# Kernel tuning notes

Hardware: AMD Instinct MI355X
Metric: run time of the kernel (lower is better)

## Reference

```python
import jax, jax.numpy as jnp
import numpy as np

N = 100_000      # nodes
E = 1_600_000    # edges (before self-loops)
IN_DIM = 128
HID = 64
NEG_SLOPE = 0.2  # PyG GATConv default


def gat_layer(x, src, dst, W, att_src, att_dst, bias, heads, out_ch):
    """PyG-style GATConv: messages flow src -> dst, softmax over incoming edges of dst."""
    n = x.shape[0]
    h = (x @ W).reshape(n, heads, out_ch)                 # [N,H,C]
    a_src = jnp.einsum('nhc,hc->nh', h, att_src)          # [N,H]
    a_dst = jnp.einsum('nhc,hc->nh', h, att_dst)          # [N,H]
    e = jax.nn.leaky_relu(a_src[src] + a_dst[dst], NEG_SLOPE)  # [E,H]
    # segment softmax over edges grouped by destination node
    m = jax.ops.segment_max(e, dst, num_segments=n)       # [N,H]
    ex = jnp.exp(e - m[dst])                              # [E,H]
    denom = jax.ops.segment_sum(ex, dst, num_segments=n)  # [N,H]
    alpha = ex / denom[dst]                               # [E,H]
    msg = alpha[:, :, None] * h[src]                      # [E,H,C]
    out = jax.ops.segment_sum(msg, dst, num_segments=n)   # [N,H,C]
    return out.reshape(n, heads * out_ch) + bias


def setup_inputs() -> dict:
    key = jax.random.key(0)
    ks = jax.random.split(key, 12)
    s = 0.1
    x = jax.random.normal(ks[0], (N, IN_DIM), jnp.float32)
    edge_index = jax.random.randint(ks[1], (2, E), 0, N, dtype=jnp.int32)
    # conv1: in_dim -> hidden, heads=2 (concat)
    W1 = jax.random.normal(ks[2], (IN_DIM, 2 * HID), jnp.float32) * s
    att_src1 = jax.random.normal(ks[3], (2, HID), jnp.float32) * s
    att_dst1 = jax.random.normal(ks[4], (2, HID), jnp.float32) * s
    b1 = jnp.zeros((2 * HID,), jnp.float32)
    # conv2: 2*hidden -> 1, heads=1
    W2 = jax.random.normal(ks[5], (2 * HID, 1), jnp.float32) * s
    att_src2 = jax.random.normal(ks[6], (1, 1), jnp.float32) * s
    att_dst2 = jax.random.normal(ks[7], (1, 1), jnp.float32) * s
    b2 = jnp.zeros((1,), jnp.float32)
    return {"x": x, "edge_index": edge_index,
            "W1": W1, "att_src1": att_src1, "att_dst1": att_dst1, "b1": b1,
            "W2": W2, "att_src2": att_src2, "att_dst2": att_dst2, "b2": b2}


def reference(x, edge_index, W1, att_src1, att_dst1, b1, W2, att_src2, att_dst2, b2):
    n = x.shape[0]
    # PyG GATConv default: add self-loops
    loop = jnp.arange(n, dtype=edge_index.dtype)
    src = jnp.concatenate([edge_index[0], loop])
    dst = jnp.concatenate([edge_index[1], loop])
    h = jax.nn.relu(gat_layer(x, src, dst, W1, att_src1, att_dst1, b1, heads=2, out_ch=HID))
    out = gat_layer(h, src, dst, W2, att_src2, att_dst2, b2, heads=1, out_ch=1)
    return jax.nn.sigmoid(out)  # [N,1]
```

## Files before the change

### kernel.cpp

```cpp
#include <hip/hip_runtime.h>
#include <hip/hip_bf16.h>
#include <hip/hip_fp8.h>
#include <hip/hip_fp16.h>

#define NEG 0.2f
#define CAP 48
#define TILE 2048
typedef unsigned int u32;
typedef unsigned short u16;
typedef unsigned char u8;
typedef unsigned long long u64;
typedef __attribute__((ext_vector_type(8))) short s8v;
typedef __attribute__((ext_vector_type(4))) float f4v;
typedef __attribute__((ext_vector_type(2))) float f2v;

__global__ __launch_bounds__(256) void binA_k(const int* __restrict__ ei,
                                              int2* __restrict__ meta,
                                              u64* __restrict__ slabs,
                                              int E, int Etot, int NB, int ntiles){
  __shared__ int bcnt[512], sc[512], bcur[512];
  int tile = blockIdx.x, tid = threadIdx.x;
  int base = tile*TILE;
  int cnt = min(TILE, Etot - base);
  for (int i=tid;i<512;i+=256) bcnt[i]=0;
  __syncthreads();
  int dd[8], ss[8];
  #pragma unroll
  for (int j=0;j<8;j++){
    int i = tid + j*256;
    if (i < cnt){
      int e = base+i;
      int d = (e<E)? ei[E+e] : e-E;
      int s = (e<E)? ei[e]   : d;
      dd[j] = d; ss[j] = s;
      atomicAdd(&bcnt[d>>8], 1);
    } else dd[j] = -1;
  }
  __syncthreads();
  sc[tid]     = bcnt[tid];
  sc[tid+256] = bcnt[tid+256];
  __syncthreads();
  for (int o=1;o<512;o<<=1){
    int i0=tid, i1=tid+256;
    int r0 = (i0>=o)? sc[i0-o]:0;
    int r1 = (i1>=o)? sc[i1-o]:0;
    __syncthreads();
    sc[i0]+=r0; sc[i1]+=r1;
    __syncthreads();
  }
  bcur[tid]     = sc[tid]     - bcnt[tid];
  bcur[tid+256] = sc[tid+256] - bcnt[tid+256];
  __syncthreads();
  for (int b=tid;b<NB;b+=256)
    meta[(size_t)b*ntiles + tile] = make_int2(sc[b]-bcnt[b], bcnt[b]);
  #pragma unroll
  for (int j=0;j<8;j++){
    if (dd[j] >= 0){
      int p = atomicAdd(&bcur[dd[j]>>8], 1);
      slabs[(size_t)base + p] = ((u64)(u32)dd[j] << 32) | (u32)ss[j];
    }
  }
}

__global__ __launch_bounds__(1024) void binB_k(const u64* __restrict__ slabs,
                                               const int2* __restrict__ meta,
                                               const float2* __restrict__ as1,
                                               const float2* __restrict__ ad1,
                                               int* __restrict__ cur,
                                               u32* __restrict__ woff,
                                               u64* __restrict__ combo,
                                               float2* __restrict__ den,
                                               int N, int ntiles){
  __shared__ u64 lcombo[CAP*256];
  __shared__ int lcnt[256], loff[256];
  __shared__ float sden0[256], sden1[256];
  __shared__ float2 sad[256];
  int b = blockIdx.x, tid = threadIdx.x;
  int lo = b<<8;
  int nn = min(256, N-lo);
  if (tid < 256){
    lcnt[tid]=0; sden0[tid]=0.f; sden1[tid]=0.f;
    sad[tid] = (tid<nn)? ad1[lo+tid] : make_float2(0.f,0.f);
  }
  __syncthreads();
  int grp = tid>>3, l8 = tid&7;
  const int2* mrow = meta + (size_t)b*ntiles;
  int2 m = (grp < ntiles)? mrow[grp] : make_int2(0,0);
  for (int t=grp; t<ntiles; t+=128){
    int2 mn = (t+128 < ntiles)? mrow[t+128] : make_int2(0,0);
    const u64* sp = slabs + (size_t)t*TILE + m.x;
    for (int i=l8; i<m.y; i+=8){
      u64 pk = sp[i];
      int d = (int)(pk>>32), s = (int)(u32)pk;
      int dl = d & 255;
      float2 av = as1[s];
      float2 adv = sad[dl];
      float e0 = av.x+adv.x; e0 = (e0>0.f)? e0 : NEG*e0;
      float e1 = av.y+adv.y; e1 = (e1>0.f)? e1 : NEG*e1;
      __half2 hw = __floats2half2_rn(__expf(e0), __expf(e1));
      float2 wr = __half22float2(hw);
      atomicAdd(&sden0[dl], wr.x);
      atomicAdd(&sden1[dl], wr.y);
      int p = atomicAdd(&lcnt[dl], 1);
      u32 wb32 = *(u32*)&hw;
      if (p < CAP) lcombo[p*256 + dl] = ((u64)wb32 << 32) | (u32)s;
    }
    m = mn;
  }
  __syncthreads();
  if (tid < 256){
    lcnt[tid] = min(lcnt[tid], CAP);
    loff[tid] = lcnt[tid];
  }
  __syncthreads();
  for (int o=1;o<256;o<<=1){
    int v = 0;
    if (tid < 256 && tid >= o) v = loff[tid-o];
    __syncthreads();
    if (tid < 256) loff[tid] += v;
    __syncthreads();
  }
  u32 wbase = (u32)b * (256u*CAP);
  {
    int g = tid>>2, q = tid&3;
    int dg  = lcnt[g];
    u32 ob  = wbase + (u32)(loff[g] - dg);
    for (int k=q; k<dg; k+=4)
      combo[(size_t)(ob + (u32)k)] = lcombo[k*256 + g];
  }
  __syncthreads();
  if (tid < nn){
    cur[lo+tid]  = lcnt[tid];
    woff[lo+tid] = wbase + (u32)(loff[tid] - lcnt[tid]);
    den[lo+tid]  = make_float2(sden0[tid], sden1[tid]);
  }
}

__global__ __launch_bounds__(256) void wt_k(const float* __restrict__ W, u16* __restrict__ Wt){
  int g = blockIdx.x*256 + threadIdx.x;
  int k = g >> 7, c = g & 127;
  __hip_bfloat16 b = __float2bfloat16(W[g]);
  Wt[c*128 + k] = *(u16*)&b;
}

__global__ __launch_bounds__(256) void gemm_k(const float* __restrict__ x,
                                              const u16* __restrict__ Wt,
                                              const float* __restrict__ aw_s,
                                              const float* __restrict__ aw_d,
                                              u8*  __restrict__ h1f,
                                              float2* __restrict__ as1,
                                              float2* __restrict__ ad1, int N){
  __shared__ u16 xs[128*136];
  __shared__ u16 ws[128*136];
  int tid = threadIdx.x;
  int rowBase = blockIdx.x * 128;
  #pragma unroll
  for (int i=0;i<16;i++){
    int j = i*256 + tid;
    int c = j >> 5, k4 = j & 31;
    *(uint2*)&ws[c*136 + k4*4] = ((const uint2*)Wt)[j];
  }
  #pragma unroll
  for (int i=0;i<16;i++){
    int j = i*256 + tid;
    int r = j >> 5, c4 = j & 31;
    float4 v = make_float4(0.f,0.f,0.f,0.f);
    if (rowBase + r < N) v = ((const float4*)x)[(size_t)(rowBase+r)*32 + c4];
    __hip_bfloat16 b0=__float2bfloat16(v.x), b1=__float2bfloat16(v.y);
    __hip_bfloat16 b2=__float2bfloat16(v.z), b3=__float2bfloat16(v.w);
    u32 w0 = (u32)*(u16*)&b0 | ((u32)*(u16*)&b1 << 16);
    u32 w1 = (u32)*(u16*)&b2 | ((u32)*(u16*)&b3 << 16);
    *(uint2*)&xs[r*136 + c4*4] = make_uint2(w0, w1);
  }
  __syncthreads();
  int wv = tid >> 6, lane = tid & 63;
  int lr = lane & 15, lk = lane >> 4;
  f4v acc[2][8];
  #pragma unroll
  for (int rt=0;rt<2;rt++)
    #pragma unroll
    for (int ct=0;ct<8;ct++) acc[rt][ct] = (f4v){0.f,0.f,0.f,0.f};
  #pragma unroll
  for (int ks=0; ks<4; ks++){
    int koff = ks*32 + lk*8;
    s8v bfrag[8];
    #pragma unroll
    for (int ct=0; ct<8; ct++)
      bfrag[ct] = *(s8v*)&ws[(ct*16 + lr)*136 + koff];
    #pragma unroll
    for (int rt=0; rt<2; rt++){
      int row = wv*32 + rt*16 + lr;
      s8v afrag = *(s8v*)&xs[row*136 + koff];
      #pragma unroll
      for (int ct=0; ct<8; ct++)
        acc[rt][ct] = __builtin_amdgcn_mfma_f32_16x16x32_bf16(afrag, bfrag[ct], acc[rt][ct], 0,0,0);
    }
  }
  #pragma unroll
  for (int rt=0; rt<2; rt++){
    float lps0[4]={0,0,0,0}, lps1[4]={0,0,0,0}, lpd0[4]={0,0,0,0}, lpd1[4]={0,0,0,0};
    int nodeB = rowBase + wv*32 + rt*16 + lk*4;
    #pragma unroll
    for (int ct=0; ct<8; ct++){
      int ch = ct*16 + lr;
      float aws = aw_s[ch], awd = aw_d[ch];
      #pragma unroll
      for (int reg=0; reg<4; reg++){
        float v = acc[rt][ct][reg];
        if (ct < 4){ lps0[reg] = fmaf(v, aws, lps0[reg]); lpd0[reg] = fmaf(v, awd, lpd0[reg]); }
        else       { lps1[reg] = fmaf(v, aws, lps1[reg]); lpd1[reg] = fmaf(v, awd, lpd1[reg]); }
      }
      int pk01 = __builtin_amdgcn_cvt_pk_fp8_f32(acc[rt][ct][0], acc[rt][ct][1], 0, false);
      int pk23 = __builtin_amdgcn_cvt_pk_fp8_f32(acc[rt][ct][2], acc[rt][ct][3], 0, false);
      if (nodeB + 0 < N) h1f[(size_t)(nodeB+0)*128 + ch] = (u8)(pk01 & 0xff);
      if (nodeB + 1 < N) h1f[(size_t)(nodeB+1)*128 + ch] = (u8)((pk01 >> 8) & 0xff);
      if (nodeB + 2 < N) h1f[(size_t)(nodeB+2)*128 + ch] = (u8)(pk23 & 0xff);
      if (nodeB + 3 < N) h1f[(size_t)(nodeB+3)*128 + ch] = (u8)((pk23 >> 8) & 0xff);
    }
    #pragma unroll
    for (int reg=0; reg<4; reg++){
      float a=lps0[reg], b=lps1[reg], c=lpd0[reg], d=lpd1[reg];
      #pragma unroll
      for (int o=1;o<16;o<<=1){
        a += __shfl_xor(a,o); b += __shfl_xor(b,o);
        c += __shfl_xor(c,o); d += __shfl_xor(d,o);
      }
      int node = nodeB + reg;
      if (lr == 0 && node < N){
        as1[node] = make_float2(a, b);
        ad1[node] = make_float2(c, d);
      }
    }
  }
}

__global__ __launch_bounds__(256) void agg1_k(const uint2* __restrict__ h1f2,
                                              const u64* __restrict__ combo,
                                              const u32* __restrict__ woff,
                                              const float2* __restrict__ den,
                                              const int* __restrict__ cur,
                                              const float4* __restrict__ b1_4,
                                              const float4* __restrict__ W2_4,
                                              float* __restrict__ h2, int N){
  int w = threadIdx.x >> 6, l = threadIdx.x & 63;
  int g = l >> 4, li = l & 15;
  int n = blockIdx.x*16 + w*4 + g;
  if (n >= N) return;
  int deg = min(cur[n], CAP);
  u32 base = woff[n];
  bool hsel = (li >= 8);
  float2 dn = den[n];
  float rd = 1.f / (hsel ? dn.y : dn.x);
  float ac0=0.f,ac1=0.f,ac2=0.f,ac3=0.f,ac4=0.f,ac5=0.f,ac6=0.f,ac7=0.f;
  for (int kk = 0; kk < deg; kk += 8){
    u64 pk[8]; bool vd[8];
    #pragma unroll
    for (int j=0;j<8;j++){
      int idx = kk + j;
      vd[j] = idx < deg;
      pk[j] = combo[(size_t)(base + (u32)(vd[j] ? idx : 0))];
    }
    uint2 hv[8];
    #pragma unroll
    for (int j=0;j<8;j++){
      u32 off = ((u32)(pk[j] & 0xffffffffu) << 4) | (u32)li;
      hv[j] = h1f2[off];
    }
    #pragma unroll
    for (int j=0;j<8;j++){
      u32 wb = (u32)(pk[j] >> 32);
      __half2 hw = *(__half2*)&wb;
      float2 wf = __half22float2(hw);
      float gw = hsel ? wf.y : wf.x;
      gw = vd[j] ? gw : 0.f;
      f2v p0 = __builtin_amdgcn_cvt_pk_f32_fp8((int)hv[j].x, false);
      f2v p1 = __builtin_amdgcn_cvt_pk_f32_fp8((int)hv[j].x, true);
      f2v p2 = __builtin_amdgcn_cvt_pk_f32_fp8((int)hv[j].y, false);
      f2v p3 = __builtin_amdgcn_cvt_pk_f32_fp8((int)hv[j].y, true);
      ac0 = fmaf(gw, p0.x, ac0); ac1 = fmaf(gw, p0.y, ac1);
      ac2 = fmaf(gw, p1.x, ac2); ac3 = fmaf(gw, p1.y, ac3);
      ac4 = fmaf(gw, p2.x, ac4); ac5 = fmaf(gw, p2.y, ac5);
      ac6 = fmaf(gw, p3.x, ac6); ac7 = fmaf(gw, p3.y, ac7);
    }
  }
  float4 bb0 = b1_4[li*2], bb1 = b1_4[li*2+1];
  float4 ww0 = W2_4[li*2], ww1 = W2_4[li*2+1];
  float p = 0.f;
  p = fmaf(fmaxf(fmaf(ac0, rd, bb0.x), 0.f), ww0.x, p);
  p = fmaf(fmaxf(fmaf(ac1, rd, bb0.y), 0.f), ww0.y, p);
  p = fmaf(fmaxf(fmaf(ac2, rd, bb0.z), 0.f), ww0.z, p);
  p = fmaf(fmaxf(fmaf(ac3, rd, bb0.w), 0.f), ww0.w, p);
  p = fmaf(fmaxf(fmaf(ac4, rd, bb1.x), 0.f), ww1.x, p);
  p = fmaf(fmaxf(fmaf(ac5, rd, bb1.y), 0.f), ww1.y, p);
  p = fmaf(fmaxf(fmaf(ac6, rd, bb1.z), 0.f), ww1.z, p);
  p = fmaf(fmaxf(fmaf(ac7, rd, bb1.w), 0.f), ww1.w, p);
  #pragma unroll
  for (int o=1;o<16;o<<=1) p += __shfl_xor(p,o);
  if (li == 0) h2[n] = p;
}

__global__ __launch_bounds__(256) void agg2_k(const float* __restrict__ h2,
                                              const int* __restrict__ cur,
                                              const u32* __restrict__ woff,
                                              const u64* __restrict__ combo,
                                              const float* __restrict__ att_s2,
                                              const float* __restrict__ att_d2,
                                              const float* __restrict__ b2,
                                              float* __restrict__ out, int N){
  int w = threadIdx.x >> 6, l = threadIdx.x & 63;
  int n = blockIdx.x*4 + w;
  if (n >= N) return;
  float as2 = att_s2[0], ad2 = att_d2[0];
  float hd = h2[n]*ad2;
  int deg = min(cur[n], CAP);
  u32 base = woff[n];
  bool v = l < deg;
  int s = (int)(u32)(combo[(size_t)(base + (u32)(v ? l : 0))] & 0xffffffffu);
  float hs = h2[s];
  float e = fmaf(hs, as2, hd); e = (e>0.f)? e : NEG*e;
  float xv = v ? __expf(e) : 0.f;
  float den = xv, wsum = xv*hs;
  #pragma unroll
  for (int o=32;o>0;o>>=1){ den += __shfl_xor(den,o); wsum += __shfl_xor(wsum,o); }
  if (l == 0){
    float z = wsum/den + b2[0];
    out[n] = 1.f/(1.f + __expf(-z));
  }
}

extern "C" void kernel_launch(void* const* d_in, const int* in_sizes, int n_in,
                              void* d_out, int out_size, void* d_ws, size_t ws_size,
                              hipStream_t stream){
  const float* x     = (const float*)d_in[0];
  const int*   ei    = (const int*)d_in[1];
  const float* W1    = (const float*)d_in[2];
  const float* aw_s  = (const float*)d_in[3];
  const float* aw_d  = (const float*)d_in[4];
  const float* b1    = (const float*)d_in[5];
  const float* W2    = (const float*)d_in[6];
  const float* at_s2 = (const float*)d_in[7];
  const float* at_d2 = (const float*)d_in[8];
  const float* b2    = (const float*)d_in[9];
  float* out = (float*)d_out;

  const int N = in_sizes[0]/128;
  const int E = in_sizes[1]/2;
  const int Etot = E + N;
  const int ntiles = (Etot + TILE - 1) / TILE;
  const int NB = (N + 255) >> 8;

  auto align256 = [](size_t v){ return (v + 255) & ~(size_t)255; };
  char* w = (char*)d_ws;
  u8* h1f       = (u8*)w;     w += align256((size_t)N*128);
  float2* as1   = (float2*)w; w += align256((size_t)N*8);
  float2* ad1   = (float2*)w; w += align256((size_t)N*8);
  float* h2     = (float*)w;  w += align256((size_t)N*4);
  int* cur      = (int*)w;    w += align256((size_t)N*4);
  u32* woff     = (u32*)w;    w += align256((size_t)N*4);
  float2* den   = (float2*)w; w += align256((size_t)N*8);
  u16* Wt       = (u16*)w;    w += align256((size_t)128*128*2);
  u64* combo    = (u64*)w;    w += align256((size_t)NB*256*CAP*8);
  u64* slabs    = (u64*)w;    w += align256((size_t)ntiles*TILE*8);
  int2* meta    = (int2*)w;   w += align256((size_t)NB*ntiles*8);

  const int tb = 256;
  binA_k<<<ntiles, tb, 0, stream>>>(ei, meta, slabs, E, Etot, NB, ntiles);
  wt_k<<<64, tb, 0, stream>>>(W1, Wt);
  gemm_k<<<(N+127)/128, tb, 0, stream>>>(x, Wt, aw_s, aw_d, h1f, as1, ad1, N);
  binB_k<<<NB, 1024, 0, stream>>>(slabs, meta, as1, ad1, cur, woff, combo, den, N, ntiles);
  agg1_k<<<(N+15)/16, tb, 0, stream>>>((const uint2*)h1f, combo, woff, den, cur,
                                       (const float4*)b1, (const float4*)W2, h2, N);
  agg2_k<<<(N+3)/4, tb, 0, stream>>>(h2, cur, woff, combo, at_s2, at_d2, b2, out, N);
}
```

Measured before the change: 174.0 us.

## Compute edge attention weights in binning pass, derive softmax denominator in aggregation

The exp-leaky-relu edge weight is now computed in binA_k, which is moved after the GEMM. The weight is packed into the slab word along with the local destination and a 24-bit source index. binB_k becomes a pure scatter into per-node slots, with no as1 gathers, no shared-memory float atomics and no den output. agg1_k sums the denominator from the weights it already reads. This trades shared atomics and a separate den array for an extra random ad1 gather per edge in binA. The denominator now covers only the first CAP edges kept per node, which changes numerics for nodes with more than CAP incoming edges.

```diff
diff --git a/kernel.cpp b/kernel.cpp
--- a/kernel.cpp
+++ b/kernel.cpp
@@ -15,6 +15,8 @@
 typedef __attribute__((ext_vector_type(2))) float f2v;
 
 __global__ __launch_bounds__(256) void binA_k(const int* __restrict__ ei,
+                                              const float2* __restrict__ as1,
+                                              const float2* __restrict__ ad1,
                                               int2* __restrict__ meta,
                                               u64* __restrict__ slabs,
                                               int E, int Etot, int NB, int ntiles){
@@ -36,6 +38,18 @@
       atomicAdd(&bcnt[d>>8], 1);
     } else dd[j] = -1;
   }
+  u32 wreg[8];
+  #pragma unroll
+  for (int j=0;j<8;j++){
+    if (dd[j] >= 0){
+      float2 av = as1[ss[j]];
+      float2 adv = ad1[dd[j]];
+      float e0 = av.x+adv.x; e0 = (e0>0.f)? e0 : NEG*e0;
+      float e1 = av.y+adv.y; e1 = (e1>0.f)? e1 : NEG*e1;
+      __half2 hw = __floats2half2_rn(__expf(e0), __expf(e1));
+      wreg[j] = *(u32*)&hw;
+    }
+  }
   __syncthreads();
   sc[tid]     = bcnt[tid];
   sc[tid+256] = bcnt[tid+256];
@@ -57,31 +71,23 @@
   for (int j=0;j<8;j++){
     if (dd[j] >= 0){
       int p = atomicAdd(&bcur[dd[j]>>8], 1);
-      slabs[(size_t)base + p] = ((u64)(u32)dd[j] << 32) | (u32)ss[j];
+      slabs[(size_t)base + p] = ((u64)wreg[j] << 32) | ((u64)(dd[j]&255) << 24) | (u32)ss[j];
     }
   }
 }
 
 __global__ __launch_bounds__(1024) void binB_k(const u64* __restrict__ slabs,
                                                const int2* __restrict__ meta,
-                                               const float2* __restrict__ as1,
-                                               const float2* __restrict__ ad1,
                                                int* __restrict__ cur,
                                                u32* __restrict__ woff,
                                                u64* __restrict__ combo,
-                                               float2* __restrict__ den,
                                                int N, int ntiles){
   __shared__ u64 lcombo[CAP*256];
   __shared__ int lcnt[256], loff[256];
-  __shared__ float sden0[256], sden1[256];
-  __shared__ float2 sad[256];
   int b = blockIdx.x, tid = threadIdx.x;
   int lo = b<<8;
   int nn = min(256, N-lo);
-  if (tid < 256){
-    lcnt[tid]=0; sden0[tid]=0.f; sden1[tid]=0.f;
-    sad[tid] = (tid<nn)? ad1[lo+tid] : make_float2(0.f,0.f);
-  }
+  if (tid < 256) lcnt[tid]=0;
   __syncthreads();
   int grp = tid>>3, l8 = tid&7;
   const int2* mrow = meta + (size_t)b*ntiles;
@@ -91,19 +97,10 @@
     const u64* sp = slabs + (size_t)t*TILE + m.x;
     for (int i=l8; i<m.y; i+=8){
       u64 pk = sp[i];
-      int d = (int)(pk>>32), s = (int)(u32)pk;
-      int dl = d & 255;
-      float2 av = as1[s];
-      float2 adv = sad[dl];
-      float e0 = av.x+adv.x; e0 = (e0>0.f)? e0 : NEG*e0;
-      float e1 = av.y+adv.y; e1 = (e1>0.f)? e1 : NEG*e1;
-      __half2 hw = __floats2half2_rn(__expf(e0), __expf(e1));
-      float2 wr = __half22float2(hw);
-      atomicAdd(&sden0[dl], wr.x);
-      atomicAdd(&sden1[dl], wr.y);
+      int dl = (int)((pk >> 24) & 255);
+      u32 s  = (u32)(pk & 0xffffff);
       int p = atomicAdd(&lcnt[dl], 1);
-      u32 wb32 = *(u32*)&hw;
-      if (p < CAP) lcombo[p*256 + dl] = ((u64)wb32 << 32) | (u32)s;
+      if (p < CAP) lcombo[p*256 + dl] = (pk & 0xffffffff00000000ull) | s;
     }
     m = mn;
   }
@@ -132,7 +129,6 @@
   if (tid < nn){
     cur[lo+tid]  = lcnt[tid];
     woff[lo+tid] = wbase + (u32)(loff[tid] - lcnt[tid]);
-    den[lo+tid]  = make_float2(sden0[tid], sden1[tid]);
   }
 }
 
@@ -237,7 +233,6 @@
 __global__ __launch_bounds__(256) void agg1_k(const uint2* __restrict__ h1f2,
                                               const u64* __restrict__ combo,
                                               const u32* __restrict__ woff,
-                                              const float2* __restrict__ den,
                                               const int* __restrict__ cur,
                                               const float4* __restrict__ b1_4,
                                               const float4* __restrict__ W2_4,
@@ -249,8 +244,7 @@
   int deg = min(cur[n], CAP);
   u32 base = woff[n];
   bool hsel = (li >= 8);
-  float2 dn = den[n];
-  float rd = 1.f / (hsel ? dn.y : dn.x);
+  float den = 0.f;
   float ac0=0.f,ac1=0.f,ac2=0.f,ac3=0.f,ac4=0.f,ac5=0.f,ac6=0.f,ac7=0.f;
   for (int kk = 0; kk < deg; kk += 8){
     u64 pk[8]; bool vd[8];
@@ -273,6 +267,7 @@
       float2 wf = __half22float2(hw);
       float gw = hsel ? wf.y : wf.x;
       gw = vd[j] ? gw : 0.f;
+      den += gw;
       f2v p0 = __builtin_amdgcn_cvt_pk_f32_fp8((int)hv[j].x, false);
       f2v p1 = __builtin_amdgcn_cvt_pk_f32_fp8((int)hv[j].x, true);
       f2v p2 = __builtin_amdgcn_cvt_pk_f32_fp8((int)hv[j].y, false);
@@ -283,6 +278,7 @@
       ac6 = fmaf(gw, p3.x, ac6); ac7 = fmaf(gw, p3.y, ac7);
     }
   }
+  float rd = 1.f / den;
   float4 bb0 = b1_4[li*2], bb1 = b1_4[li*2+1];
   float4 ww0 = W2_4[li*2], ww1 = W2_4[li*2+1];
   float p = 0.f;
@@ -357,18 +353,17 @@
   float* h2     = (float*)w;  w += align256((size_t)N*4);
   int* cur      = (int*)w;    w += align256((size_t)N*4);
   u32* woff     = (u32*)w;    w += align256((size_t)N*4);
-  float2* den   = (float2*)w; w += align256((size_t)N*8);
   u16* Wt       = (u16*)w;    w += align256((size_t)128*128*2);
   u64* combo    = (u64*)w;    w += align256((size_t)NB*256*CAP*8);
   u64* slabs    = (u64*)w;    w += align256((size_t)ntiles*TILE*8);
   int2* meta    = (int2*)w;   w += align256((size_t)NB*ntiles*8);
 
   const int tb = 256;
-  binA_k<<<ntiles, tb, 0, stream>>>(ei, meta, slabs, E, Etot, NB, ntiles);
   wt_k<<<64, tb, 0, stream>>>(W1, Wt);
   gemm_k<<<(N+127)/128, tb, 0, stream>>>(x, Wt, aw_s, aw_d, h1f, as1, ad1, N);
-  binB_k<<<NB, 1024, 0, stream>>>(slabs, meta, as1, ad1, cur, woff, combo, den, N, ntiles);
-  agg1_k<<<(N+15)/16, tb, 0, stream>>>((const uint2*)h1f, combo, woff, den, cur,
+  binA_k<<<ntiles, tb, 0, stream>>>(ei, as1, ad1, meta, slabs, E, Etot, NB, ntiles);
+  binB_k<<<NB, 1024, 0, stream>>>(slabs, meta, cur, woff, combo, N, ntiles);
+  agg1_k<<<(N+15)/16, tb, 0, stream>>>((const uint2*)h1f, combo, woff, cur,
                                        (const float4*)b1, (const float4*)W2, h2, N);
   agg2_k<<<(N+3)/4, tb, 0, stream>>>(h2, cur, woff, combo, at_s2, at_d2, b2, out, N);
 }
```

After: 165.6 us. -4.8%, faster.
